# Optimization experiments

Measured on AMD Instinct MI355X. Metric: run time of the kernel, lower is better.

## Reference

```python
import jax, jax.numpy as jnp
import numpy as np

EMBED_DIM = 1024
NUM_HEADS = 16
HEAD_DIM = EMBED_DIM // NUM_HEADS


def setup_inputs() -> dict:
    key = jax.random.key(0)
    k_h, k_q, k_k, k_v, k_o = jax.random.split(key, 5)
    scale = 1.0 / np.sqrt(EMBED_DIM)
    return {
        "h": jax.random.normal(k_h, (2, 2048, EMBED_DIM), dtype=jnp.float32),
        "W_q": jax.random.normal(k_q, (EMBED_DIM, EMBED_DIM), dtype=jnp.float32) * scale,
        "W_k": jax.random.normal(k_k, (EMBED_DIM, EMBED_DIM), dtype=jnp.float32) * scale,
        "W_v": jax.random.normal(k_v, (EMBED_DIM, EMBED_DIM), dtype=jnp.float32) * scale,
        "W_o": jax.random.normal(k_o, (EMBED_DIM, EMBED_DIM), dtype=jnp.float32) * scale,
    }


def reference(h, W_q, W_k, W_v, W_o):
    B, S, E = h.shape
    H, D = NUM_HEADS, HEAD_DIM
    # nn.Linear stores weight as [out, in]; y = x @ W.T
    q = (h @ W_q.T).reshape(B, S, H, D).transpose(0, 2, 1, 3)  # [B,H,S,D]
    k = (h @ W_k.T).reshape(B, S, H, D).transpose(0, 2, 1, 3)
    v = (h @ W_v.T).reshape(B, S, H, D).transpose(0, 2, 1, 3)
    scores = jnp.einsum("bhsd,bhtd->bhst", q, k) / np.sqrt(D)
    attn = jax.nn.softmax(scores, axis=-1)
    ctx = jnp.einsum("bhst,bhtd->bhsd", attn, v)  # [B,H,S,D]
    ctx = ctx.transpose(0, 2, 1, 3).reshape(B, S, E)
    return ctx @ W_o.T
```

## Files before the change

kernel.cpp:

```cpp
#include <hip/hip_runtime.h>
#include <hip/hip_bf16.h>

#define B_ 2
#define S_ 2048
#define E_ 1024
#define H_ 16
#define D_ 64
#define M_ (B_*S_)

typedef __attribute__((ext_vector_type(8))) short bf16x8;
typedef __attribute__((ext_vector_type(4))) float f32x4;
typedef __attribute__((ext_vector_type(8))) unsigned short u16x8;
typedef __attribute__((ext_vector_type(4))) unsigned short u16x4;

__device__ __forceinline__ unsigned short f2bf_hw(float f) {
  union { __hip_bfloat16 h; unsigned short u; } c;
  c.h = __float2bfloat16(f);
  return c.u;
}

__device__ __forceinline__ void gload_lds16(const void* g, void* l) {
  __builtin_amdgcn_global_load_lds(
      (const __attribute__((address_space(1))) void*)g,
      (__attribute__((address_space(3))) void*)l, 16, 0, 0);
}

__global__ __launch_bounds__(256) void cvt_all(const float* __restrict__ h,
                                               const float* __restrict__ Wq,
                                               const float* __restrict__ Wk,
                                               const float* __restrict__ Wv,
                                               const float* __restrict__ Wo,
                                               unsigned short* __restrict__ dst,
                                               float qscale) {
  int i = blockIdx.x * 256 + threadIdx.x;
  const float4* src4;
  int idx;
  float scale = 1.f;
  if (i < (1 << 20)) {
    src4 = (const float4*)h; idx = i;
  } else {
    int t = i - (1 << 20);
    int j = t >> 18;
    idx = t & ((1 << 18) - 1);
    src4 = (const float4*)((j == 0) ? Wq : (j == 1) ? Wk : (j == 2) ? Wv : Wo);
    if (j == 0) scale = qscale;
  }
  float4 v = src4[idx];
  u16x4 o;
  o[0] = f2bf_hw(v.x * scale);
  o[1] = f2bf_hw(v.y * scale);
  o[2] = f2bf_hw(v.z * scale);
  o[3] = f2bf_hw(v.w * scale);
  ((u16x4*)dst)[i] = o;
}

template<int OUT_BF16>
__device__ __forceinline__ void gemm_body64(const unsigned short* __restrict__ A,
                                            const unsigned short* __restrict__ W,
                                            void* __restrict__ Cv,
                                            int row0, int col0, int N, int K,
                                            unsigned short* As, unsigned short* Bs) {
  const int tid = threadIdx.x;
  const int lane = tid & 63, wave = tid >> 6;
  const int wr = wave >> 1, wc = wave & 1;
  const int lq = lane & 15, lg = lane >> 4;
  f32x4 acc[4][4] = {};

  for (int kt = 0; kt < K; kt += 64) {
#pragma unroll
    for (int i = 0; i < 4; ++i) {
      int t = tid + i * 256;
      int rr = t >> 3;
      int sch = (t & 7) ^ (rr & 7);
      gload_lds16(A + (size_t)(row0 + rr) * K + kt + sch * 8, &As[t * 8]);
      gload_lds16(W + (size_t)(col0 + rr) * K + kt + sch * 8, &Bs[t * 8]);
    }
    __syncthreads();
#pragma unroll
    for (int ks = 0; ks < 2; ++ks) {
      bf16x8 af[4], bfr[4];
#pragma unroll
      for (int mi = 0; mi < 4; ++mi) {
        int row = wr * 64 + mi * 16 + lq;
        af[mi] = *(const bf16x8*)&As[row * 64 + (((ks * 4 + lg) ^ (row & 7))) * 8];
      }
#pragma unroll
      for (int ni = 0; ni < 4; ++ni) {
        int row = wc * 64 + ni * 16 + lq;
        bfr[ni] = *(const bf16x8*)&Bs[row * 64 + (((ks * 4 + lg) ^ (row & 7))) * 8];
      }
#pragma unroll
      for (int mi = 0; mi < 4; ++mi)
#pragma unroll
        for (int ni = 0; ni < 4; ++ni)
          acc[mi][ni] = __builtin_amdgcn_mfma_f32_16x16x32_bf16(af[mi], bfr[ni], acc[mi][ni], 0, 0, 0);
    }
    __syncthreads();
  }

#pragma unroll
  for (int mi = 0; mi < 4; ++mi)
#pragma unroll
    for (int ni = 0; ni < 4; ++ni) {
      int row = row0 + wr * 64 + mi * 16 + lg * 4;
      int col = col0 + wc * 64 + ni * 16 + lq;
#pragma unroll
      for (int r = 0; r < 4; ++r) {
        float v = acc[mi][ni][r];
        if (OUT_BF16) ((unsigned short*)Cv)[(size_t)(row + r) * N + col] = f2bf_hw(v);
        else          ((float*)Cv)[(size_t)(row + r) * N + col] = v;
      }
    }
}

__global__ __launch_bounds__(256) void gemm_qkv(const unsigned short* __restrict__ A,
                                                const unsigned short* __restrict__ Wq,
                                                const unsigned short* __restrict__ Wk,
                                                const unsigned short* __restrict__ Wv,
                                                unsigned short* __restrict__ Qb,
                                                unsigned short* __restrict__ Kb,
                                                unsigned short* __restrict__ Vb) {
  __shared__ unsigned short As[128 * 64];
  __shared__ unsigned short Bs[128 * 64];
  const int mat = blockIdx.y >> 3;
  const int col0 = (blockIdx.y & 7) * 128;
  const unsigned short* W = (mat == 0) ? Wq : (mat == 1) ? Wk : Wv;
  unsigned short* C = (mat == 0) ? Qb : (mat == 1) ? Kb : Vb;
  gemm_body64<1>(A, W, C, blockIdx.x * 128, col0, E_, E_, As, Bs);
}

__global__ __launch_bounds__(256) void gemm_out(const unsigned short* __restrict__ A,
                                                const unsigned short* __restrict__ W,
                                                float* __restrict__ C) {
  __shared__ unsigned short As[64 * 64];
  __shared__ unsigned short Bs[128 * 64];
  const int tid = threadIdx.x;
  const int lane = tid & 63, wave = tid >> 6;
  const int wr = wave >> 1, wc = wave & 1;
  const int lq = lane & 15, lg = lane >> 4;
  const int row0 = blockIdx.x * 64, col0 = blockIdx.y * 128;
  const int N = E_, K = E_;
  f32x4 acc[2][4] = {};

  for (int kt = 0; kt < K; kt += 64) {
#pragma unroll
    for (int i = 0; i < 2; ++i) {
      int t = tid + i * 256;
      int rr = t >> 3;
      int sch = (t & 7) ^ (rr & 7);
      gload_lds16(A + (size_t)(row0 + rr) * K + kt + sch * 8, &As[t * 8]);
    }
#pragma unroll
    for (int i = 0; i < 4; ++i) {
      int t = tid + i * 256;
      int rr = t >> 3;
      int sch = (t & 7) ^ (rr & 7);
      gload_lds16(W + (size_t)(col0 + rr) * K + kt + sch * 8, &Bs[t * 8]);
    }
    __syncthreads();
#pragma unroll
    for (int ks = 0; ks < 2; ++ks) {
      bf16x8 af[2], bfr[4];
#pragma unroll
      for (int mi = 0; mi < 2; ++mi) {
        int row = wr * 32 + mi * 16 + lq;
        af[mi] = *(const bf16x8*)&As[row * 64 + (((ks * 4 + lg) ^ (row & 7))) * 8];
      }
#pragma unroll
      for (int ni = 0; ni < 4; ++ni) {
        int row = wc * 64 + ni * 16 + lq;
        bfr[ni] = *(const bf16x8*)&Bs[row * 64 + (((ks * 4 + lg) ^ (row & 7))) * 8];
      }
#pragma unroll
      for (int mi = 0; mi < 2; ++mi)
#pragma unroll
        for (int ni = 0; ni < 4; ++ni)
          acc[mi][ni] = __builtin_amdgcn_mfma_f32_16x16x32_bf16(af[mi], bfr[ni], acc[mi][ni], 0, 0, 0);
    }
    __syncthreads();
  }

#pragma unroll
  for (int mi = 0; mi < 2; ++mi)
#pragma unroll
    for (int ni = 0; ni < 4; ++ni) {
      int row = row0 + wr * 32 + mi * 16 + lg * 4;
      int col = col0 + wc * 64 + ni * 16 + lq;
#pragma unroll
      for (int r = 0; r < 4; ++r)
        C[(size_t)(row + r) * N + col] = acc[mi][ni][r];
    }
}

__global__ __launch_bounds__(256) void transpose_v(const unsigned short* __restrict__ V,
                                                   unsigned short* __restrict__ VT) {
  __shared__ unsigned short tile[64][72];
  const int tid = threadIdx.x;
  const int s0 = blockIdx.x * 64;
  const int h = blockIdx.y;
  const int b = blockIdx.z;
  const int r = tid >> 3;
  const int c = (tid & 7) * 8;
  const unsigned short* src = V + ((size_t)(b * S_) + s0) * E_ + h * 64;
#pragma unroll
  for (int i = 0; i < 2; ++i) {
    int rr = r + i * 32;
    u16x8 v = *(const u16x8*)(src + (size_t)rr * E_ + c);
#pragma unroll
    for (int j = 0; j < 8; ++j) tile[rr][c + j] = v[j];
  }
  __syncthreads();
  unsigned short* dst = VT + ((size_t)((b * H_ + h) * 64)) * S_ + s0;
#pragma unroll
  for (int i = 0; i < 2; ++i) {
    int d = r + i * 32;
    u16x8 o;
#pragma unroll
    for (int j = 0; j < 8; ++j) o[j] = tile[c + j][d];
    *(u16x8*)(dst + (size_t)d * S_ + c) = o;
  }
}

__global__ __launch_bounds__(256) void attn(const unsigned short* __restrict__ Q,
                                            const unsigned short* __restrict__ K,
                                            const unsigned short* __restrict__ VT,
                                            unsigned short* __restrict__ ctx) {
  __shared__ unsigned short Ks[64 * 64];
  __shared__ unsigned short Vs[64 * 64];
  __shared__ unsigned short Ps[4][16 * 72];
  const int tid = threadIdx.x, lane = tid & 63, wave = tid >> 6;
  const int lq = lane & 15, lg = lane >> 4;
  const int bh = blockIdx.y, b = bh >> 4, h = bh & 15;
  const int q0 = blockIdx.x * 64;

  const unsigned short* Qbase = Q + ((size_t)(b * S_) + q0 + wave * 16 + lq) * E_ + h * 64;
  bf16x8 qf0 = *(const bf16x8*)(Qbase + lg * 8);
  bf16x8 qf1 = *(const bf16x8*)(Qbase + 32 + lg * 8);
  const unsigned short* Kbase = K + (size_t)(b * S_) * E_ + h * 64;
  const unsigned short* Vtb = VT + (size_t)((b * H_ + h) * 64) * S_;
  unsigned short* Pw = Ps[wave];

  f32x4 oacc[4] = {};
  float m_run = -1e30f, l_run = 0.f;

  for (int kc = 0; kc < S_; kc += 64) {
    __syncthreads();
#pragma unroll
    for (int i = 0; i < 2; ++i) {
      int tt = tid + i * 256;
      int r = tt >> 3;
      int sch = (tt & 7) ^ (r & 7);
      gload_lds16(Kbase + (size_t)(kc + r) * E_ + sch * 8, &Ks[tt * 8]);
      gload_lds16(Vtb + (size_t)r * S_ + kc + sch * 8, &Vs[tt * 8]);
    }
    __syncthreads();

    f32x4 st[4] = {};
    __builtin_amdgcn_s_setprio(1);
#pragma unroll
    for (int mf = 0; mf < 4; ++mf) {
      int row = mf * 16 + lq;
      bf16x8 kf0 = *(const bf16x8*)&Ks[row * 64 + ((lg ^ (row & 7)) * 8)];
      bf16x8 kf1 = *(const bf16x8*)&Ks[row * 64 + (((4 + lg) ^ (row & 7)) * 8)];
      st[mf] = __builtin_amdgcn_mfma_f32_16x16x32_bf16(kf0, qf0, st[mf], 0, 0, 0);
      st[mf] = __builtin_amdgcn_mfma_f32_16x16x32_bf16(kf1, qf1, st[mf], 0, 0, 0);
    }
    __builtin_amdgcn_s_setprio(0);

    float c0 = fmaxf(fmaxf(st[0][0], st[0][1]), fmaxf(st[0][2], st[0][3]));
    float c1 = fmaxf(fmaxf(st[1][0], st[1][1]), fmaxf(st[1][2], st[1][3]));
    float c2 = fmaxf(fmaxf(st[2][0], st[2][1]), fmaxf(st[2][2], st[2][3]));
    float c3 = fmaxf(fmaxf(st[3][0], st[3][1]), fmaxf(st[3][2], st[3][3]));
    float cm = fmaxf(fmaxf(c0, c1), fmaxf(c2, c3));
    cm = fmaxf(cm, __shfl_xor(cm, 16));
    cm = fmaxf(cm, __shfl_xor(cm, 32));

    if (!__all(cm - m_run <= 8.f)) {
      float m_new = fmaxf(m_run, cm);
      float alpha = __builtin_amdgcn_exp2f(m_run - m_new);
#pragma unroll
      for (int r = 0; r < 4; ++r) {
        float ar = __shfl(alpha, lg * 4 + r);
#pragma unroll
        for (int nf = 0; nf < 4; ++nf) oacc[nf][r] *= ar;
      }
      l_run *= alpha;
      m_run = m_new;
    }

    float ls = 0.f;
#pragma unroll
    for (int mf = 0; mf < 4; ++mf) {
      u16x4 pb;
#pragma unroll
      for (int r = 0; r < 4; ++r) {
        float p = __builtin_amdgcn_exp2f(st[mf][r] - m_run);
        ls += p;
        pb[r] = f2bf_hw(p);
      }
      *(u16x4*)&Pw[lq * 72 + mf * 16 + lg * 4] = pb;
    }
    ls += __shfl_xor(ls, 16);
    ls += __shfl_xor(ls, 32);
    l_run += ls;
    asm volatile("s_waitcnt lgkmcnt(0)" ::: "memory");

    __builtin_amdgcn_s_setprio(1);
#pragma unroll
    for (int ks = 0; ks < 2; ++ks) {
      bf16x8 pf = *(const bf16x8*)&Pw[lq * 72 + ks * 32 + lg * 8];
#pragma unroll
      for (int nf = 0; nf < 4; ++nf) {
        int row = nf * 16 + lq;
        bf16x8 vf = *(const bf16x8*)&Vs[row * 64 + (((ks * 4 + lg) ^ (row & 7)) * 8)];
        oacc[nf] = __builtin_amdgcn_mfma_f32_16x16x32_bf16(pf, vf, oacc[nf], 0, 0, 0);
      }
    }
    __builtin_amdgcn_s_setprio(0);
  }

#pragma unroll
  for (int r = 0; r < 4; ++r) {
    float lr = __shfl(l_run, lg * 4 + r);
    float inv = 1.f / lr;
#pragma unroll
    for (int nf = 0; nf < 4; ++nf) {
      ctx[((size_t)(b * S_) + q0 + wave * 16 + lg * 4 + r) * E_ + h * 64 + nf * 16 + lq] =
          f2bf_hw(oacc[nf][r] * inv);
    }
  }
}

extern "C" void kernel_launch(void* const* d_in, const int* in_sizes, int n_in,
                              void* d_out, int out_size, void* d_ws, size_t ws_size,
                              hipStream_t stream) {
  const float* h  = (const float*)d_in[0];
  const float* Wq = (const float*)d_in[1];
  const float* Wk = (const float*)d_in[2];
  const float* Wv = (const float*)d_in[3];
  const float* Wo = (const float*)d_in[4];
  float* out = (float*)d_out;
  char* ws = (char*)d_ws;

  const size_t SZ_H = (size_t)M_ * E_ * 2;
  const size_t SZ_W = (size_t)E_ * E_ * 2;
  unsigned short* hb  = (unsigned short*)(ws);
  unsigned short* wqb = (unsigned short*)(ws + SZ_H);
  unsigned short* wkb = (unsigned short*)(ws + SZ_H + SZ_W);
  unsigned short* wvb = (unsigned short*)(ws + SZ_H + 2 * SZ_W);
  unsigned short* wob = (unsigned short*)(ws + SZ_H + 3 * SZ_W);
  unsigned short* Qb  = (unsigned short*)(ws + SZ_H + 4 * SZ_W);
  unsigned short* Kb  = (unsigned short*)(ws + 2 * SZ_H + 4 * SZ_W);
  unsigned short* Vb  = (unsigned short*)(ws + 3 * SZ_H + 4 * SZ_W);
  unsigned short* VTb = hb;
  unsigned short* Cb  = Vb;

  const float QSCALE = 0.125f * 1.44269504f;
  cvt_all<<<8192, 256, 0, stream>>>(h, Wq, Wk, Wv, Wo, hb, QSCALE);

  gemm_qkv<<<dim3(M_ / 128, 3 * E_ / 128), 256, 0, stream>>>(hb, wqb, wkb, wvb, Qb, Kb, Vb);

  transpose_v<<<dim3(S_ / 64, H_, B_), 256, 0, stream>>>(Vb, VTb);

  attn<<<dim3(S_ / 64, B_ * H_), 256, 0, stream>>>(Qb, Kb, VTb, Cb);

  gemm_out<<<dim3(M_ / 64, E_ / 128), 256, 0, stream>>>(Cb, wob, out);
}
```

Before: 209.5 us.

## Double-buffer K tiles in attention and swizzle block order in all kernels

The attention kernel now double-buffers K in LDS, prefetching the next K tile during the current QK^T/softmax. V staging is issued after the PV MFMAs so its load overlaps the next tile's score computation, with explicit vmcnt waits and raw barriers replacing __syncthreads. Block indices in the QKV GEMM, output GEMM and attention kernels are remapped with a stride-8 swizzle to change which tiles run concurrently, aiming at better L2 locality. This adds LDS usage and relies on hand-counted vmcnt values, which is fragile if the compiler reorders or adds loads.

```diff
diff --git a/kernel.cpp b/kernel.cpp
--- a/kernel.cpp
+++ b/kernel.cpp
@@ -24,6 +24,9 @@
       (const __attribute__((address_space(1))) void*)g,
       (__attribute__((address_space(3))) void*)l, 16, 0, 0);
 }
+
+#define BARRIER() do { asm volatile("" ::: "memory"); \
+  __builtin_amdgcn_s_barrier(); asm volatile("" ::: "memory"); } while (0)
 
 __global__ __launch_bounds__(256) void cvt_all(const float* __restrict__ h,
                                                const float* __restrict__ Wq,
@@ -122,11 +125,14 @@
                                                 unsigned short* __restrict__ Vb) {
   __shared__ unsigned short As[128 * 64];
   __shared__ unsigned short Bs[128 * 64];
-  const int mat = blockIdx.y >> 3;
-  const int col0 = (blockIdx.y & 7) * 128;
+  int lin = blockIdx.x + 32 * blockIdx.y;
+  int sw = (lin & 7) * 96 + (lin >> 3);
+  int bx = sw & 31, by = sw >> 5;
+  const int mat = by >> 3;
+  const int col0 = (by & 7) * 128;
   const unsigned short* W = (mat == 0) ? Wq : (mat == 1) ? Wk : Wv;
   unsigned short* C = (mat == 0) ? Qb : (mat == 1) ? Kb : Vb;
-  gemm_body64<1>(A, W, C, blockIdx.x * 128, col0, E_, E_, As, Bs);
+  gemm_body64<1>(A, W, C, bx * 128, col0, E_, E_, As, Bs);
 }
 
 __global__ __launch_bounds__(256) void gemm_out(const unsigned short* __restrict__ A,
@@ -138,7 +144,9 @@
   const int lane = tid & 63, wave = tid >> 6;
   const int wr = wave >> 1, wc = wave & 1;
   const int lq = lane & 15, lg = lane >> 4;
-  const int row0 = blockIdx.x * 64, col0 = blockIdx.y * 128;
+  int lin = blockIdx.x + 64 * blockIdx.y;
+  int sw = (lin & 7) * 64 + (lin >> 3);
+  const int row0 = (sw & 63) * 64, col0 = (sw >> 6) * 128;
   const int N = E_, K = E_;
   f32x4 acc[2][4] = {};
 
@@ -225,13 +233,15 @@
                                             const unsigned short* __restrict__ K,
                                             const unsigned short* __restrict__ VT,
                                             unsigned short* __restrict__ ctx) {
-  __shared__ unsigned short Ks[64 * 64];
+  __shared__ unsigned short Ks[2][64 * 64];
   __shared__ unsigned short Vs[64 * 64];
   __shared__ unsigned short Ps[4][16 * 72];
   const int tid = threadIdx.x, lane = tid & 63, wave = tid >> 6;
   const int lq = lane & 15, lg = lane >> 4;
-  const int bh = blockIdx.y, b = bh >> 4, h = bh & 15;
-  const int q0 = blockIdx.x * 64;
+  int lin = blockIdx.x + 32 * blockIdx.y;
+  int sw = (lin & 7) * 128 + (lin >> 3);
+  const int bh = sw >> 5, b = bh >> 4, h = bh & 15;
+  const int q0 = (sw & 31) * 64;
 
   const unsigned short* Qbase = Q + ((size_t)(b * S_) + q0 + wave * 16 + lq) * E_ + h * 64;
   bf16x8 qf0 = *(const bf16x8*)(Qbase + lg * 8);
@@ -240,28 +250,45 @@
   const unsigned short* Vtb = VT + (size_t)((b * H_ + h) * 64) * S_;
   unsigned short* Pw = Ps[wave];
 
-  f32x4 oacc[4] = {};
-  float m_run = -1e30f, l_run = 0.f;
-
-  for (int kc = 0; kc < S_; kc += 64) {
-    __syncthreads();
+  auto STAGE_K = [&](int buf, int kc) {
 #pragma unroll
     for (int i = 0; i < 2; ++i) {
       int tt = tid + i * 256;
       int r = tt >> 3;
       int sch = (tt & 7) ^ (r & 7);
-      gload_lds16(Kbase + (size_t)(kc + r) * E_ + sch * 8, &Ks[tt * 8]);
+      gload_lds16(Kbase + (size_t)(kc + r) * E_ + sch * 8, &Ks[buf][tt * 8]);
+    }
+  };
+  auto STAGE_V = [&](int kc) {
+#pragma unroll
+    for (int i = 0; i < 2; ++i) {
+      int tt = tid + i * 256;
+      int r = tt >> 3;
+      int sch = (tt & 7) ^ (r & 7);
       gload_lds16(Vtb + (size_t)r * S_ + kc + sch * 8, &Vs[tt * 8]);
     }
-    __syncthreads();
+  };
+
+  f32x4 oacc[4] = {};
+  float m_run = -1e30f, l_run = 0.f;
+
+  STAGE_K(0, 0);
+  asm volatile("s_waitcnt vmcnt(0)" ::: "memory");
+  BARRIER();
+  STAGE_V(0);
+
+  int cur = 0;
+  for (int kc = 0; kc < S_; kc += 64) {
+    const bool pref = (kc + 64 < S_);
+    if (pref) STAGE_K(cur ^ 1, kc + 64);
 
     f32x4 st[4] = {};
     __builtin_amdgcn_s_setprio(1);
 #pragma unroll
     for (int mf = 0; mf < 4; ++mf) {
       int row = mf * 16 + lq;
-      bf16x8 kf0 = *(const bf16x8*)&Ks[row * 64 + ((lg ^ (row & 7)) * 8)];
-      bf16x8 kf1 = *(const bf16x8*)&Ks[row * 64 + (((4 + lg) ^ (row & 7)) * 8)];
+      bf16x8 kf0 = *(const bf16x8*)&Ks[cur][row * 64 + ((lg ^ (row & 7)) * 8)];
+      bf16x8 kf1 = *(const bf16x8*)&Ks[cur][row * 64 + (((4 + lg) ^ (row & 7)) * 8)];
       st[mf] = __builtin_amdgcn_mfma_f32_16x16x32_bf16(kf0, qf0, st[mf], 0, 0, 0);
       st[mf] = __builtin_amdgcn_mfma_f32_16x16x32_bf16(kf1, qf1, st[mf], 0, 0, 0);
     }
@@ -305,6 +332,10 @@
     l_run += ls;
     asm volatile("s_waitcnt lgkmcnt(0)" ::: "memory");
 
+    if (pref) asm volatile("s_waitcnt vmcnt(2)" ::: "memory");
+    else      asm volatile("s_waitcnt vmcnt(0)" ::: "memory");
+    BARRIER();
+
     __builtin_amdgcn_s_setprio(1);
 #pragma unroll
     for (int ks = 0; ks < 2; ++ks) {
@@ -317,6 +348,13 @@
       }
     }
     __builtin_amdgcn_s_setprio(0);
+
+    if (pref) {
+      asm volatile("s_waitcnt vmcnt(0)" ::: "memory");
+      BARRIER();
+      STAGE_V(kc + 64);
+      cur ^= 1;
+    }
   }
 
 #pragma unroll
```

Result: slower. 214.4 us (+2.4%).
